# Optimization experiments

Hardware: AMD Instinct MI355X
Metric: run time of the kernel (lower is better)

Reference implementation:

```python
import jax, jax.numpy as jnp
import numpy as np

KH, KW = 79, 69
STD = 5.0


def setup_inputs() -> dict:
    key = jax.random.key(0)
    x = jax.random.normal(key, (32, 512, 512, 1), dtype=jnp.float32)
    return {"x": x}


def reference(x):
    # Uniform 79x69 box filter (constant, not learned), SAME padding, stride 1.
    filt = jnp.full((KH, KW, 1, 1), 1.0 / (KH * KW), dtype=x.dtype)
    mean = jax.lax.conv_general_dilated(
        x, filt,
        window_strides=(1, 1),
        padding='SAME',
        dimension_numbers=('NHWC', 'HWIO', 'NHWC'),
    )
    return (x - mean) / jnp.asarray(STD, dtype=x.dtype)
```

## Files before the change

### kernel.cpp

```cpp
#include <hip/hip_runtime.h>


#define HH   512
#define WW   512
#define NIMG 32
#define RH   39
#define RW   34
#define TH   32
#define SPAN (TH + 2*RH)
#define LDSW 584
#define NT   1024

__device__ __forceinline__ float hsum4(float4 v) { return (v.x + v.y) + (v.z + v.w); }

template<bool INT>
__device__ __forceinline__ float ldv(const float* col, int g) {
    if (INT) return col[(size_t)g * WW];
    return (g >= 0 && g < HH) ? col[(size_t)g * WW] : 0.0f;
}

template<bool INT, int T0, int N>
__device__ __forceinline__ void silent2(const float* cA, const float* cB, int gbase,
                                        float& SA, float& SB) {
    float a0 = 0, a1 = 0, b0 = 0, b1 = 0;
    #pragma unroll
    for (int i = 0; i + 2 <= N; i += 2) {
        a0 += ldv<INT>(cA, gbase + T0 + i);
        b0 += ldv<INT>(cB, gbase + T0 + i);
        a1 += ldv<INT>(cA, gbase + T0 + i + 1);
        b1 += ldv<INT>(cB, gbase + T0 + i + 1);
    }
    if (N & 1) {
        a0 += ldv<INT>(cA, gbase + T0 + N - 1);
        b0 += ldv<INT>(cB, gbase + T0 + N - 1);
    }
    SA = a0 + a1; SB = b0 + b1;
}

template<bool INT, int T0, int N>
__device__ __forceinline__ void walk_up_write(float (*cs)[LDSW], const float* cA,
                                              const float* cB, int gbase,
                                              int lA, int lB, float SA, float SB) {
    #pragma unroll
    for (int t = T0; t < T0 + N; ++t) {
        SA += ldv<INT>(cA, gbase + t);
        SB += ldv<INT>(cB, gbase + t);
        cs[t - 78][lA] = SA;
        cs[t - 78][lB] = SB;
    }
}

template<bool INT, int T1, int N>
__device__ __forceinline__ void walk_dn_add(float (*cs)[LDSW], const float* cA,
                                            const float* cB, int gbase,
                                            int lA, int lB, float SA, float SB) {
    #pragma unroll
    for (int t = T1; t > T1 - N; --t) {
        SA += ldv<INT>(cA, gbase + t);
        SB += ldv<INT>(cB, gbase + t);
        cs[t][lA] += SA;
        cs[t][lB] += SB;
    }
}

template<bool INT>
__device__ __forceinline__ void phase1(float (*cs)[LDSW], const float* img,
                                       int gbase, int tid) {
    int q  = tid >> 8;
    int cg = tid & 255;
    const float* cA = img + cg;
    const float* cB = img + cg + 256;
    int lA = 34 + cg, lB = 34 + cg + 256;

    float SA, SB;
    if (q == 0)      silent2<INT, 16, 39>(cA, cB, gbase, SA, SB);
    else if (q == 1) silent2<INT, 32, 23>(cA, cB, gbase, SA, SB);
    else if (q == 2) silent2<INT, 55, 23>(cA, cB, gbase, SA, SB);
    else             silent2<INT, 55, 39>(cA, cB, gbase, SA, SB);

    for (int i = tid; i < TH * 72; i += NT) {
        int r = i / 72, c = i - r * 72;
        cs[r][c < 34 ? c : 512 + c] = 0.0f;
    }

    if (q == 2)      walk_up_write<INT, 78, 16>(cs, cA, cB, gbase, lA, lB, SA, SB);
    else if (q == 3) walk_up_write<INT, 94, 16>(cs, cA, cB, gbase, lA, lB, SA, SB);
    __syncthreads();
    if (q == 0)      walk_dn_add<INT, 15, 16>(cs, cA, cB, gbase, lA, lB, SA, SB);
    else if (q == 1) walk_dn_add<INT, 31, 16>(cs, cA, cB, gbase, lA, lB, SA, SB);
    __syncthreads();
}

__global__ __launch_bounds__(NT, 8) void fused_kernel(const float* __restrict__ x,
                                                      float* __restrict__ out) {
    __shared__ float cs[TH][LDSW];

    int d   = blockIdx.x;
    int lin = (d & 7) * 64 + (d >> 3);
    int n   = lin >> 4;
    int h0  = (lin & 15) * TH;
    int tid = threadIdx.x;

    const float* img = x + (size_t)n * HH * WW;
    int gbase = h0 - RH;

    if (gbase >= 0 && gbase + SPAN <= HH) phase1<true >(cs, img, gbase, tid);
    else                                  phase1<false>(cs, img, gbase, tid);

    const float INV = 1.0f / (79.0f * 69.0f);
    int row = tid >> 5;
    int c0  = (tid & 31) * 16;

    const float4* cp = (const float4*)(&cs[row][0] + c0);
    const float4* xp = (const float4*)(img + (size_t)(h0 + row) * WW + c0);
    float4*       op = (float4*)(out + (size_t)n * HH * WW
                                     + (size_t)(h0 + row) * WW + c0);

    float4 xin0 = xp[0], xin1 = xp[1], xin2 = xp[2], xin3 = xp[3];

    float4 t4 = make_float4(0, 0, 0, 0), u4 = make_float4(0, 0, 0, 0);
    #pragma unroll
    for (int i = 0; i < 16; i += 2) {
        float4 a = cp[i], b = cp[i + 1];
        t4.x += a.x; t4.y += a.y; t4.z += a.z; t4.w += a.w;
        u4.x += b.x; u4.y += b.y; u4.z += b.z; u4.w += b.w;
    }
    float T = hsum4(t4) + hsum4(u4) + hsum4(cp[16]);

    float4 xin[4] = { xin0, xin1, xin2, xin3 };
    #pragma unroll
    for (int g = 0; g < 4; ++g) {
        float4 vin  = cp[17 + g];
        float4 vout = cp[g];
        float pin0 = vin.x,  pin1 = pin0 + vin.y,
              pin2 = pin1 + vin.z, pin3 = pin2 + vin.w;
        float po0  = vout.x, po1 = po0 + vout.y,
              po2  = po1 + vout.z, po3 = po2 + vout.w;

        float4 xi = xin[g];
        float4 o;
        o.x = (xi.x - (T + pin0)       * INV) * 0.2f;
        o.y = (xi.y - (T + pin1 - po0) * INV) * 0.2f;
        o.z = (xi.z - (T + pin2 - po1) * INV) * 0.2f;
        o.w = (xi.w - (T + pin3 - po2) * INV) * 0.2f;
        op[g] = o;

        T += pin3 - po3;
    }
}

extern "C" void kernel_launch(void* const* d_in, const int* in_sizes, int n_in,
                              void* d_out, int out_size, void* d_ws, size_t ws_size,
                              hipStream_t stream) {
    const float* x   = (const float*)d_in[0];
    float*       out = (float*)d_out;

    int nblocks = NIMG * (HH / TH);
    fused_kernel<<<nblocks, NT, 0, stream>>>(x, out);
}
```

Before: 107.3 us.

## Compute full vertical column sums per thread with one column each at 512 threads

```diff
diff --git a/kernel.cpp b/kernel.cpp
--- a/kernel.cpp
+++ b/kernel.cpp
@@ -7,9 +7,9 @@
 #define RH   39
 #define RW   34
 #define TH   32
-#define SPAN (TH + 2*RH)
+#define SPAN 110
 #define LDSW 584
-#define NT   1024
+#define NT   512
 
 __device__ __forceinline__ float hsum4(float4 v) { return (v.x + v.y) + (v.z + v.w); }
 
@@ -19,79 +19,57 @@
     return (g >= 0 && g < HH) ? col[(size_t)g * WW] : 0.0f;
 }
 
-template<bool INT, int T0, int N>
-__device__ __forceinline__ void silent2(const float* cA, const float* cB, int gbase,
-                                        float& SA, float& SB) {
-    float a0 = 0, a1 = 0, b0 = 0, b1 = 0;
+template<bool INT>
+__device__ __forceinline__ void phase1(float (*cs)[LDSW], const float* img,
+                                       int gbase, int c) {
+    const float* col = img + c;
+
+    float lo[32];
     #pragma unroll
-    for (int i = 0; i + 2 <= N; i += 2) {
-        a0 += ldv<INT>(cA, gbase + T0 + i);
-        b0 += ldv<INT>(cB, gbase + T0 + i);
-        a1 += ldv<INT>(cA, gbase + T0 + i + 1);
-        b1 += ldv<INT>(cB, gbase + T0 + i + 1);
+    for (int t = 0; t < 32; ++t) lo[t] = ldv<INT>(col, gbase + t);
+
+    float m0 = 0, m1 = 0, m2 = 0, m3 = 0;
+    #pragma unroll
+    for (int t = 32; t < 52; t += 4) {
+        m0 += ldv<INT>(col, gbase + t + 0);
+        m1 += ldv<INT>(col, gbase + t + 1);
+        m2 += ldv<INT>(col, gbase + t + 2);
+        m3 += ldv<INT>(col, gbase + t + 3);
     }
-    if (N & 1) {
-        a0 += ldv<INT>(cA, gbase + T0 + N - 1);
-        b0 += ldv<INT>(cB, gbase + T0 + N - 1);
+    m0 += ldv<INT>(col, gbase + 52);
+    m1 += ldv<INT>(col, gbase + 53);
+    m2 += ldv<INT>(col, gbase + 54);
+    float M = (m0 + m1) + (m2 + m3);
+
+    float hi[32];
+    #pragma unroll
+    for (int t = 0; t < 32; ++t) hi[t] = ldv<INT>(col, gbase + 78 + t);
+
+    float u0 = 0, u1 = 0, u2 = 0, u3 = 0;
+    #pragma unroll
+    for (int t = 55; t < 75; t += 4) {
+        u0 += ldv<INT>(col, gbase + t + 0);
+        u1 += ldv<INT>(col, gbase + t + 1);
+        u2 += ldv<INT>(col, gbase + t + 2);
+        u3 += ldv<INT>(col, gbase + t + 3);
     }
-    SA = a0 + a1; SB = b0 + b1;
-}
+    u0 += ldv<INT>(col, gbase + 75);
+    u1 += ldv<INT>(col, gbase + 76);
+    u2 += ldv<INT>(col, gbase + 77);
+    float U = (u0 + u1) + (u2 + u3);
 
-template<bool INT, int T0, int N>
-__device__ __forceinline__ void walk_up_write(float (*cs)[LDSW], const float* cA,
-                                              const float* cB, int gbase,
-                                              int lA, int lB, float SA, float SB) {
     #pragma unroll
-    for (int t = T0; t < T0 + N; ++t) {
-        SA += ldv<INT>(cA, gbase + t);
-        SB += ldv<INT>(cB, gbase + t);
-        cs[t - 78][lA] = SA;
-        cs[t - 78][lB] = SB;
+    for (int k = 0; k < 32; ++k) { U += hi[k]; hi[k] = U; }
+
+    float L = M;
+    #pragma unroll
+    for (int k = 31; k >= 0; --k) {
+        L += lo[k];
+        cs[k][34 + c] = L + hi[k];
     }
 }
 
-template<bool INT, int T1, int N>
-__device__ __forceinline__ void walk_dn_add(float (*cs)[LDSW], const float* cA,
-                                            const float* cB, int gbase,
-                                            int lA, int lB, float SA, float SB) {
-    #pragma unroll
-    for (int t = T1; t > T1 - N; --t) {
-        SA += ldv<INT>(cA, gbase + t);
-        SB += ldv<INT>(cB, gbase + t);
-        cs[t][lA] += SA;
-        cs[t][lB] += SB;
-    }
-}
-
-template<bool INT>
-__device__ __forceinline__ void phase1(float (*cs)[LDSW], const float* img,
-                                       int gbase, int tid) {
-    int q  = tid >> 8;
-    int cg = tid & 255;
-    const float* cA = img + cg;
-    const float* cB = img + cg + 256;
-    int lA = 34 + cg, lB = 34 + cg + 256;
-
-    float SA, SB;
-    if (q == 0)      silent2<INT, 16, 39>(cA, cB, gbase, SA, SB);
-    else if (q == 1) silent2<INT, 32, 23>(cA, cB, gbase, SA, SB);
-    else if (q == 2) silent2<INT, 55, 23>(cA, cB, gbase, SA, SB);
-    else             silent2<INT, 55, 39>(cA, cB, gbase, SA, SB);
-
-    for (int i = tid; i < TH * 72; i += NT) {
-        int r = i / 72, c = i - r * 72;
-        cs[r][c < 34 ? c : 512 + c] = 0.0f;
-    }
-
-    if (q == 2)      walk_up_write<INT, 78, 16>(cs, cA, cB, gbase, lA, lB, SA, SB);
-    else if (q == 3) walk_up_write<INT, 94, 16>(cs, cA, cB, gbase, lA, lB, SA, SB);
-    __syncthreads();
-    if (q == 0)      walk_dn_add<INT, 15, 16>(cs, cA, cB, gbase, lA, lB, SA, SB);
-    else if (q == 1) walk_dn_add<INT, 31, 16>(cs, cA, cB, gbase, lA, lB, SA, SB);
-    __syncthreads();
-}
-
-__global__ __launch_bounds__(NT, 8) void fused_kernel(const float* __restrict__ x,
+__global__ __launch_bounds__(NT, 4) void fused_kernel(const float* __restrict__ x,
                                                       float* __restrict__ out) {
     __shared__ float cs[TH][LDSW];
 
@@ -104,19 +82,27 @@
     const float* img = x + (size_t)n * HH * WW;
     int gbase = h0 - RH;
 
+    for (int i = tid; i < TH * 72; i += NT) {
+        int r = i / 72, cc = i - r * 72;
+        cs[r][cc < 34 ? cc : 512 + cc] = 0.0f;
+    }
+
     if (gbase >= 0 && gbase + SPAN <= HH) phase1<true >(cs, img, gbase, tid);
     else                                  phase1<false>(cs, img, gbase, tid);
+    __syncthreads();
 
     const float INV = 1.0f / (79.0f * 69.0f);
-    int row = tid >> 5;
-    int c0  = (tid & 31) * 16;
+    int row = tid >> 4;
+    int c0  = (tid & 15) * 32;
 
     const float4* cp = (const float4*)(&cs[row][0] + c0);
     const float4* xp = (const float4*)(img + (size_t)(h0 + row) * WW + c0);
     float4*       op = (float4*)(out + (size_t)n * HH * WW
                                      + (size_t)(h0 + row) * WW + c0);
 
-    float4 xin0 = xp[0], xin1 = xp[1], xin2 = xp[2], xin3 = xp[3];
+    float4 xin[8];
+    #pragma unroll
+    for (int i = 0; i < 8; ++i) xin[i] = xp[i];
 
     float4 t4 = make_float4(0, 0, 0, 0), u4 = make_float4(0, 0, 0, 0);
     #pragma unroll
@@ -127,9 +113,8 @@
     }
     float T = hsum4(t4) + hsum4(u4) + hsum4(cp[16]);
 
-    float4 xin[4] = { xin0, xin1, xin2, xin3 };
     #pragma unroll
-    for (int g = 0; g < 4; ++g) {
+    for (int g = 0; g < 8; ++g) {
         float4 vin  = cp[17 + g];
         float4 vout = cp[g];
         float pin0 = vin.x,  pin1 = pin0 + vin.y,
```

Result: faster. 95.50 us (-11.0%).
